# Kernel tuning notes

Hardware: AMD Instinct MI355X
Metric: run time of the kernel (lower is better)

Reference implementation:

```python
import jax, jax.numpy as jnp
import numpy as np

B, N, D = 32, 2048, 1024


def setup_inputs() -> dict:
    key0 = jax.random.key(0)
    ks = jax.random.split(key0, 9)
    scale = 1.0 / np.sqrt(D)
    query = jax.random.normal(ks[0], (B, D), dtype=jnp.float32)
    key = jax.random.normal(ks[1], (B, N, D), dtype=jnp.float32)
    mask = jax.random.randint(ks[2], (B, N), 0, 2, dtype=jnp.int32)
    W1 = jax.random.uniform(ks[3], (D, D), jnp.float32, -scale, scale)
    b1 = jax.random.uniform(ks[4], (D,), jnp.float32, -scale, scale)
    W2 = jax.random.uniform(ks[5], (D, D), jnp.float32, -scale, scale)
    b2 = jax.random.uniform(ks[6], (D,), jnp.float32, -scale, scale)
    v_w = jax.random.uniform(ks[7], (D,), jnp.float32, -scale, scale)
    v_b = jax.random.uniform(ks[8], (), jnp.float32, -scale, scale)
    return {"query": query, "key": key, "mask": mask,
            "W1": W1, "b1": b1, "W2": W2, "b2": b2, "v_w": v_w, "v_b": v_b}


def reference(query, key, mask, W1, b1, W2, b2, v_w, v_b):
    # key_out: [B, N, D] = key @ W1^T + b1 (nn.Linear convention)
    key_out = jnp.einsum('bnd,ed->bne', key, W1) + b1
    # query_out: [B, D] -> broadcast over N
    query_out = jnp.einsum('bd,ed->be', query, W2) + b2
    h = jnp.tanh(key_out + query_out[:, None, :])  # [B, N, D]
    ui = jnp.einsum('bnd,d->bn', h, v_w) + v_b      # v: D -> 1, squeezed
    ui = jnp.where(mask.astype(bool), ui, -jnp.inf)
    return ui
```

## Files before the change

kernel.cpp:

```cpp
#include <hip/hip_runtime.h>
#include <hip/hip_bf16.h>
#include <math.h>

#define B_ 32
#define N_ 2048
#define D_ 1024
#define M_ (B_ * N_)

typedef float  fx4  __attribute__((ext_vector_type(4)));
typedef __bf16 bf16x8 __attribute__((ext_vector_type(8)));
typedef unsigned short us4 __attribute__((ext_vector_type(4)));
typedef unsigned short us8 __attribute__((ext_vector_type(8)));

#define WS_T 2097152ULL

#define MASK_NEG_SENTINEL (-1.0e30f)

__device__ inline unsigned short f2b(float f) {
    __hip_bfloat16 h = __float2bfloat16(f);
    return *reinterpret_cast<unsigned short*>(&h);
}

__global__ void w1_convert_kernel(const fx4* __restrict__ W1,
                                  us4* __restrict__ w1b4) {
    int idx = blockIdx.x * blockDim.x + threadIdx.x;
#pragma unroll
    for (int i = 0; i < 4; ++i) {
        int j = idx + i * 65536;
        fx4 v = W1[j];
        us4 o; o.x = f2b(v.x); o.y = f2b(v.y); o.z = f2b(v.z); o.w = f2b(v.w);
        w1b4[j] = o;
    }
}

__global__ void tq_kernel(const float* __restrict__ query,
                          const float* __restrict__ W2,
                          const float* __restrict__ b1,
                          const float* __restrict__ b2,
                          float* __restrict__ t) {
    int tid = threadIdx.x;
    int p = blockIdx.x * 32 + (tid >> 3);
    int j = tid & 7;
    int b = p >> 10;
    int e = p & 1023;
    const fx4* q = (const fx4*)query + (size_t)b * 256;
    const fx4* w = (const fx4*)W2 + (size_t)e * 256;
    float acc = 0.f;
#pragma unroll 4
    for (int it = 0; it < 32; ++it) {
        int k4 = it * 8 + j;
        fx4 qv = q[k4];
        fx4 wv = w[k4];
        acc += qv.x * wv.x + qv.y * wv.y + qv.z * wv.z + qv.w * wv.w;
    }
    acc += __shfl_xor(acc, 1);
    acc += __shfl_xor(acc, 2);
    acc += __shfl_xor(acc, 4);
    if (j == 0) t[p] = acc + b1[e] + b2[e];
}

__device__ inline float fast_tanh(float x) {
    float ax = fabsf(x);
    float e  = __expf(-2.0f * ax);
    float r  = (1.0f - e) / (1.0f + e);
    return copysignf(r, x);
}

#define BM 64
#define WNC 64
#define NCHUNK 2

__global__ void __launch_bounds__(512)
fused_main(const float* __restrict__ key,
           const unsigned short* __restrict__ w1b,
           const float* __restrict__ t,
           const float* __restrict__ v_w,
           const float* __restrict__ v_b,
           const int* __restrict__ mask,
           float* __restrict__ out) {
    __shared__ unsigned short As[BM * D_];
    __shared__ float rs[8][BM];

    const int tid  = threadIdx.x;
    const int lane = tid & 63;
    const int wave = tid >> 6;
    const int quad = lane >> 4;
    const int l15  = lane & 15;
    const int m0   = blockIdx.x * BM;

    {
#pragma unroll
        for (int r8 = 0; r8 < 8; ++r8) {
            const int row = wave * 8 + r8;
            const fx4* src = (const fx4*)(key + (size_t)(m0 + row) * D_);
#pragma unroll
            for (int p = 0; p < 2; ++p) {
                const int s = p * 64 + lane;
                fx4 v0 = src[s * 2];
                fx4 v1 = src[s * 2 + 1];
                us8 o;
                o[0] = f2b(v0.x); o[1] = f2b(v0.y);
                o[2] = f2b(v0.z); o[3] = f2b(v0.w);
                o[4] = f2b(v1.x); o[5] = f2b(v1.y);
                o[6] = f2b(v1.z); o[7] = f2b(v1.w);
                const int ss = s ^ (row & 7);
                *(us8*)((char*)As + row * 2048 + ss * 16) = o;
            }
        }
    }
    __syncthreads();

    const int b_idx = m0 >> 11;
    const float* trow = t + (size_t)b_idx * D_;
    float rsum[4][4] = {};

    for (int c = 0; c < NCHUNK; ++c) {
        const int e0 = wave * (WNC * NCHUNK) + c * WNC;
        fx4 acc[4][4] = {};
        const unsigned short* bptr =
            w1b + (size_t)(e0 + l15) * D_ + quad * 8;

        for (int k0 = 0; k0 < D_; k0 += 32) {
            bf16x8 a[4], b[4];
#pragma unroll
            for (int j = 0; j < 4; ++j)
                b[j] = *(const bf16x8*)(bptr + (size_t)j * 16 * D_ + k0);
#pragma unroll
            for (int i = 0; i < 4; ++i) {
                const int row  = i * 16 + l15;
                const int slot = ((k0 >> 3) + quad) ^ (row & 7);
                a[i] = *(const bf16x8*)((const char*)As + row * 2048 + slot * 16);
            }
#pragma unroll
            for (int i = 0; i < 4; ++i)
#pragma unroll
                for (int j = 0; j < 4; ++j)
                    acc[i][j] = __builtin_amdgcn_mfma_f32_16x16x32_bf16(
                        a[i], b[j], acc[i][j], 0, 0, 0);
        }

        float vwv[4], tqv[4];
#pragma unroll
        for (int j = 0; j < 4; ++j) {
            const int e = e0 + j * 16 + l15;
            vwv[j] = v_w[e];
            tqv[j] = trow[e];
        }
#pragma unroll
        for (int i = 0; i < 4; ++i)
#pragma unroll
            for (int r = 0; r < 4; ++r) {
                float s = 0.f;
#pragma unroll
                for (int j = 0; j < 4; ++j)
                    s += vwv[j] * fast_tanh(acc[i][j][r] + tqv[j]);
                rsum[i][r] += s;
            }
    }

#pragma unroll
    for (int i = 0; i < 4; ++i)
#pragma unroll
        for (int r = 0; r < 4; ++r) {
            float s = rsum[i][r];
            s += __shfl_xor(s, 1);
            s += __shfl_xor(s, 2);
            s += __shfl_xor(s, 4);
            s += __shfl_xor(s, 8);
            if (l15 == 0) rs[wave][i * 16 + quad * 4 + r] = s;
        }
    __syncthreads();

    if (tid < BM) {
        float u = 0.f;
#pragma unroll
        for (int w = 0; w < 8; ++w) u += rs[w][tid];
        const int m = m0 + tid;
        out[m] = mask[m] ? (u + v_b[0]) : MASK_NEG_SENTINEL;
    }
}

extern "C" void kernel_launch(void* const* d_in, const int* in_sizes, int n_in,
                              void* d_out, int out_size, void* d_ws, size_t ws_size,
                              hipStream_t stream) {
    const float* query = (const float*)d_in[0];
    const float* key   = (const float*)d_in[1];
    const int*   mask  = (const int*)d_in[2];
    const float* W1    = (const float*)d_in[3];
    const float* b1    = (const float*)d_in[4];
    const float* W2    = (const float*)d_in[5];
    const float* b2    = (const float*)d_in[6];
    const float* v_w   = (const float*)d_in[7];
    const float* v_b   = (const float*)d_in[8];

    char* ws = (char*)d_ws;
    unsigned short* w1b = (unsigned short*)ws;
    float*          t   = (float*)(ws + WS_T);

    w1_convert_kernel<<<256, 256, 0, stream>>>((const fx4*)W1, (us4*)w1b);
    tq_kernel<<<1024, 256, 0, stream>>>(query, W2, b1, b2, t);
    fused_main<<<M_ / BM, 512, 0, stream>>>(key, w1b, t, v_w, v_b, mask,
                                            (float*)d_out);
}
```

Baseline: 627.2 us.

## Double-buffer K-slices of W1 and key in LDS with async global-to-LDS loads

Replaces the full-row key staging with a K-streamed loop that double-buffers 32-wide slices of both the bf16 W1 tile and the converted key tile in LDS. W1 slices use global_load_lds so the copy overlaps MFMA work. The block grows to 16 waves, each owning 64 output features, which removes the per-wave chunk loop. It trades per-step block-wide barriers for overlapping global latency with compute.

```diff
diff --git a/kernel.cpp b/kernel.cpp
--- a/kernel.cpp
+++ b/kernel.cpp
@@ -8,9 +8,9 @@
 #define M_ (B_ * N_)
 
 typedef float  fx4  __attribute__((ext_vector_type(4)));
+typedef float  fx2  __attribute__((ext_vector_type(2)));
 typedef __bf16 bf16x8 __attribute__((ext_vector_type(8)));
 typedef unsigned short us4 __attribute__((ext_vector_type(4)));
-typedef unsigned short us8 __attribute__((ext_vector_type(8)));
 
 #define WS_T 2097152ULL
 
@@ -67,10 +67,14 @@
 }
 
 #define BM 64
-#define WNC 64
-#define NCHUNK 2
-
-__global__ void __launch_bounds__(512)
+#define BK 32
+
+#define GLD16(g, l)                                                        \
+    __builtin_amdgcn_global_load_lds(                                      \
+        (const __attribute__((address_space(1))) void*)(g),                \
+        (__attribute__((address_space(3))) void*)(l), 16, 0, 0)
+
+__global__ void __launch_bounds__(1024, 4)
 fused_main(const float* __restrict__ key,
            const unsigned short* __restrict__ w1b,
            const float* __restrict__ t,
@@ -78,8 +82,9 @@
            const float* __restrict__ v_b,
            const int* __restrict__ mask,
            float* __restrict__ out) {
-    __shared__ unsigned short As[BM * D_];
-    __shared__ float rs[8][BM];
+    __shared__ unsigned short Bs[2][D_ * BK];
+    __shared__ unsigned short As[2][BM * BK];
+    __shared__ float rs[16][BM];
 
     const int tid  = threadIdx.x;
     const int lane = tid & 63;
@@ -88,81 +93,97 @@
     const int l15  = lane & 15;
     const int m0   = blockIdx.x * BM;
 
+    const int sB  = (lane & 7) ^ (lane >> 3);
+    const int eL  = ((lane >> 3) << 1) | (sB >> 2);
+    const int ksB = sB & 3;
+    const unsigned short* bsrc =
+        w1b + (size_t)(wave * 64 + eL) * D_ + ksB * 8;
+
+    const int arow = tid >> 4;
+    const int akk  = tid & 15;
+    const float* asrc = key + (size_t)(m0 + arow) * D_ + akk * 2;
+    const int aP  = arow >> 1;
+    const int asl = (((arow & 1) << 2) | (akk >> 2)) ^ (aP & 7);
+    const int aDstOff = aP * 128 + asl * 16 + (akk & 3) * 4;
+
+    int aOff[4], bOff[4];
+#pragma unroll
+    for (int i = 0; i < 4; ++i) {
+        int row = i * 16 + l15;
+        aOff[i] = (row >> 1) * 128 +
+                  ((((row & 1) << 2) | quad) ^ ((row >> 1) & 7)) * 16;
+    }
+#pragma unroll
+    for (int j = 0; j < 4; ++j) {
+        int e = wave * 64 + j * 16 + l15;
+        bOff[j] = (e >> 1) * 128 +
+                  ((((e & 1) << 2) | quad) ^ ((e >> 1) & 7)) * 16;
+    }
+
+    fx4 acc[4][4] = {};
+
     {
-#pragma unroll
-        for (int r8 = 0; r8 < 8; ++r8) {
-            const int row = wave * 8 + r8;
-            const fx4* src = (const fx4*)(key + (size_t)(m0 + row) * D_);
-#pragma unroll
-            for (int p = 0; p < 2; ++p) {
-                const int s = p * 64 + lane;
-                fx4 v0 = src[s * 2];
-                fx4 v1 = src[s * 2 + 1];
-                us8 o;
-                o[0] = f2b(v0.x); o[1] = f2b(v0.y);
-                o[2] = f2b(v0.z); o[3] = f2b(v0.w);
-                o[4] = f2b(v1.x); o[5] = f2b(v1.y);
-                o[6] = f2b(v1.z); o[7] = f2b(v1.w);
-                const int ss = s ^ (row & 7);
-                *(us8*)((char*)As + row * 2048 + ss * 16) = o;
-            }
+        char* bd = (char*)Bs[0] + wave * 4096;
+#pragma unroll
+        for (int q = 0; q < 4; ++q)
+            GLD16(bsrc + q * 16 * D_, bd + q * 1024);
+        fx2 v = *(const fx2*)asrc;
+        unsigned int pk = f2b(v.x) | ((unsigned int)f2b(v.y) << 16);
+        *(unsigned int*)((char*)As[0] + aDstOff) = pk;
+    }
+    __syncthreads();
+
+    int cur = 0;
+    for (int tt = 0; tt < 32; ++tt) {
+        const int k0n = (tt + 1) * BK;
+        fx2 vA;
+        const bool pf = (tt < 31);
+        if (pf) {
+            char* bd = (char*)Bs[cur ^ 1] + wave * 4096;
+#pragma unroll
+            for (int q = 0; q < 4; ++q)
+                GLD16(bsrc + q * 16 * D_ + k0n, bd + q * 1024);
+            vA = *(const fx2*)(asrc + k0n);
         }
-    }
-    __syncthreads();
-
-    const int b_idx = m0 >> 11;
-    const float* trow = t + (size_t)b_idx * D_;
-    float rsum[4][4] = {};
-
-    for (int c = 0; c < NCHUNK; ++c) {
-        const int e0 = wave * (WNC * NCHUNK) + c * WNC;
-        fx4 acc[4][4] = {};
-        const unsigned short* bptr =
-            w1b + (size_t)(e0 + l15) * D_ + quad * 8;
-
-        for (int k0 = 0; k0 < D_; k0 += 32) {
-            bf16x8 a[4], b[4];
+
+        bf16x8 a[4], b[4];
+#pragma unroll
+        for (int i = 0; i < 4; ++i)
+            a[i] = *(const bf16x8*)((const char*)As[cur] + aOff[i]);
+#pragma unroll
+        for (int j = 0; j < 4; ++j)
+            b[j] = *(const bf16x8*)((const char*)Bs[cur] + bOff[j]);
+#pragma unroll
+        for (int i = 0; i < 4; ++i)
 #pragma unroll
             for (int j = 0; j < 4; ++j)
-                b[j] = *(const bf16x8*)(bptr + (size_t)j * 16 * D_ + k0);
-#pragma unroll
-            for (int i = 0; i < 4; ++i) {
-                const int row  = i * 16 + l15;
-                const int slot = ((k0 >> 3) + quad) ^ (row & 7);
-                a[i] = *(const bf16x8*)((const char*)As + row * 2048 + slot * 16);
-            }
-#pragma unroll
-            for (int i = 0; i < 4; ++i)
-#pragma unroll
-                for (int j = 0; j < 4; ++j)
-                    acc[i][j] = __builtin_amdgcn_mfma_f32_16x16x32_bf16(
-                        a[i], b[j], acc[i][j], 0, 0, 0);
+                acc[i][j] = __builtin_amdgcn_mfma_f32_16x16x32_bf16(
+                    a[i], b[j], acc[i][j], 0, 0, 0);
+
+        if (pf) {
+            unsigned int pk = f2b(vA.x) | ((unsigned int)f2b(vA.y) << 16);
+            *(unsigned int*)((char*)As[cur ^ 1] + aDstOff) = pk;
         }
-
-        float vwv[4], tqv[4];
-#pragma unroll
-        for (int j = 0; j < 4; ++j) {
-            const int e = e0 + j * 16 + l15;
-            vwv[j] = v_w[e];
-            tqv[j] = trow[e];
-        }
-#pragma unroll
-        for (int i = 0; i < 4; ++i)
-#pragma unroll
-            for (int r = 0; r < 4; ++r) {
-                float s = 0.f;
-#pragma unroll
-                for (int j = 0; j < 4; ++j)
-                    s += vwv[j] * fast_tanh(acc[i][j][r] + tqv[j]);
-                rsum[i][r] += s;
-            }
-    }
-
+        __syncthreads();
+        cur ^= 1;
+    }
+
+    const float* trow = t + (size_t)(m0 >> 11) * D_;
+    float vwv[4], tqv[4];
+#pragma unroll
+    for (int j = 0; j < 4; ++j) {
+        int e = wave * 64 + j * 16 + l15;
+        vwv[j] = v_w[e];
+        tqv[j] = trow[e];
+    }
 #pragma unroll
     for (int i = 0; i < 4; ++i)
 #pragma unroll
         for (int r = 0; r < 4; ++r) {
-            float s = rsum[i][r];
+            float s = 0.f;
+#pragma unroll
+            for (int j = 0; j < 4; ++j)
+                s += vwv[j] * fast_tanh(acc[i][j][r] + tqv[j]);
             s += __shfl_xor(s, 1);
             s += __shfl_xor(s, 2);
             s += __shfl_xor(s, 4);
@@ -174,7 +195,7 @@
     if (tid < BM) {
         float u = 0.f;
 #pragma unroll
-        for (int w = 0; w < 8; ++w) u += rs[w][tid];
+        for (int w = 0; w < 16; ++w) u += rs[w][tid];
         const int m = m0 + tid;
         out[m] = mask[m] ? (u + v_b[0]) : MASK_NEG_SENTINEL;
     }
@@ -199,6 +220,6 @@
 
     w1_convert_kernel<<<256, 256, 0, stream>>>((const fx4*)W1, (us4*)w1b);
     tq_kernel<<<1024, 256, 0, stream>>>(query, W2, b1, b2, t);
-    fused_main<<<M_ / BM, 512, 0, stream>>>(key, w1b, t, v_w, v_b, mask,
-                                            (float*)d_out);
-}
+    fused_main<<<M_ / BM, 1024, 0, stream>>>(key, w1b, t, v_w, v_b, mask,
+                                             (float*)d_out);
+}
```

Result: no change. 618.1 us (-1.5%).

## Split D output across blocks with double-buffered K-streaming and atomic reduction

Applied to the files above, without the earlier changes.

The main kernel now has each 256-thread block compute a 64-row tile against a quarter of the output features (256 columns). It streams the key operand through two small 32-wide LDS buffers with register prefetch and bf16 conversion, and raises MFMA priority during the multiply. Per-row partial sums go to a zeroed workspace via atomicAdd, and a finalize kernel applies the mask and bias. Weight conversion, the query projection and accumulator zeroing are merged into one prep launch. This cuts LDS use per block, raising occupancy and overlapping loads with compute. The cost is that each key tile is re-read four times, plus the atomics and an extra launch.

```diff
diff --git a/kernel.cpp b/kernel.cpp
--- a/kernel.cpp
+++ b/kernel.cpp
@@ -12,7 +12,8 @@
 typedef unsigned short us4 __attribute__((ext_vector_type(4)));
 typedef unsigned short us8 __attribute__((ext_vector_type(8)));
 
-#define WS_T 2097152ULL
+#define WS_T   2097152ULL
+#define WS_ACC 2228224ULL
 
 #define MASK_NEG_SENTINEL (-1.0e30f)
 
@@ -21,42 +22,50 @@
     return *reinterpret_cast<unsigned short*>(&h);
 }
 
-__global__ void w1_convert_kernel(const fx4* __restrict__ W1,
-                                  us4* __restrict__ w1b4) {
-    int idx = blockIdx.x * blockDim.x + threadIdx.x;
-#pragma unroll
-    for (int i = 0; i < 4; ++i) {
-        int j = idx + i * 65536;
-        fx4 v = W1[j];
-        us4 o; o.x = f2b(v.x); o.y = f2b(v.y); o.z = f2b(v.z); o.w = f2b(v.w);
-        w1b4[j] = o;
-    }
-}
-
-__global__ void tq_kernel(const float* __restrict__ query,
-                          const float* __restrict__ W2,
-                          const float* __restrict__ b1,
-                          const float* __restrict__ b2,
-                          float* __restrict__ t) {
-    int tid = threadIdx.x;
-    int p = blockIdx.x * 32 + (tid >> 3);
-    int j = tid & 7;
-    int b = p >> 10;
-    int e = p & 1023;
-    const fx4* q = (const fx4*)query + (size_t)b * 256;
-    const fx4* w = (const fx4*)W2 + (size_t)e * 256;
-    float acc = 0.f;
+__global__ void prep_kernel(const fx4* __restrict__ W1,
+                            us4* __restrict__ w1b4,
+                            const float* __restrict__ query,
+                            const float* __restrict__ W2,
+                            const float* __restrict__ b1,
+                            const float* __restrict__ b2,
+                            float* __restrict__ t,
+                            fx4* __restrict__ accz) {
+    const int bid = blockIdx.x;
+    const int tid = threadIdx.x;
+    if (bid < 256) {
+        int idx = bid * 256 + tid;
+#pragma unroll
+        for (int i = 0; i < 4; ++i) {
+            int j = idx + i * 65536;
+            fx4 v = W1[j];
+            us4 o; o.x = f2b(v.x); o.y = f2b(v.y);
+            o.z = f2b(v.z); o.w = f2b(v.w);
+            w1b4[j] = o;
+        }
+    } else if (bid < 1280) {
+        int p = (bid - 256) * 32 + (tid >> 3);
+        int j = tid & 7;
+        int b = p >> 10;
+        int e = p & 1023;
+        const fx4* q = (const fx4*)query + (size_t)b * 256;
+        const fx4* w = (const fx4*)W2 + (size_t)e * 256;
+        float acc = 0.f;
 #pragma unroll 4
-    for (int it = 0; it < 32; ++it) {
-        int k4 = it * 8 + j;
-        fx4 qv = q[k4];
-        fx4 wv = w[k4];
-        acc += qv.x * wv.x + qv.y * wv.y + qv.z * wv.z + qv.w * wv.w;
-    }
-    acc += __shfl_xor(acc, 1);
-    acc += __shfl_xor(acc, 2);
-    acc += __shfl_xor(acc, 4);
-    if (j == 0) t[p] = acc + b1[e] + b2[e];
+        for (int it = 0; it < 32; ++it) {
+            int k4 = it * 8 + j;
+            fx4 qv = q[k4];
+            fx4 wv = w[k4];
+            acc += qv.x * wv.x + qv.y * wv.y + qv.z * wv.z + qv.w * wv.w;
+        }
+        acc += __shfl_xor(acc, 1);
+        acc += __shfl_xor(acc, 2);
+        acc += __shfl_xor(acc, 4);
+        if (j == 0) t[p] = acc + b1[e] + b2[e];
+    } else {
+        int idx = (bid - 1280) * 256 + tid;
+        fx4 z = {0.f, 0.f, 0.f, 0.f};
+        accz[idx] = z;
+    }
 }
 
 __device__ inline float fast_tanh(float x) {
@@ -67,102 +76,133 @@
 }
 
 #define BM 64
-#define WNC 64
-#define NCHUNK 2
-
-__global__ void __launch_bounds__(512)
+#define BK 32
+
+__global__ void __launch_bounds__(256, 3)
 fused_main(const float* __restrict__ key,
            const unsigned short* __restrict__ w1b,
            const float* __restrict__ t,
            const float* __restrict__ v_w,
-           const float* __restrict__ v_b,
-           const int* __restrict__ mask,
-           float* __restrict__ out) {
-    __shared__ unsigned short As[BM * D_];
-    __shared__ float rs[8][BM];
+           float* __restrict__ accum) {
+    __shared__ unsigned short As0[BM * BK];
+    __shared__ unsigned short As1[BM * BK];
+    __shared__ float rs[4][BM];
 
     const int tid  = threadIdx.x;
     const int lane = tid & 63;
     const int wave = tid >> 6;
     const int quad = lane >> 4;
     const int l15  = lane & 15;
-    const int m0   = blockIdx.x * BM;
+
+    const int p_ = blockIdx.x;
+    const int mt = (p_ >> 5) * 8 + (p_ & 7);
+    const int hh = (p_ >> 3) & 3;
+    const int m0 = mt * BM;
+    const int eb = hh * 256;
+
+    const unsigned short* bbase =
+        w1b + (size_t)(eb + wave * 64 + l15) * D_ + quad * 8;
+
+    const int arow = tid >> 2;
+    const int akq  = tid & 3;
+    const float* asrc = key + (size_t)(m0 + arow) * D_ + akq * 8;
+    const int aP  = arow >> 1;
+    const int asl = (((arow & 1) << 2) | akq) ^ (aP & 7);
+    const int aDstOff = aP * 128 + asl * 16;
+
+    int aOff[4];
+#pragma unroll
+    for (int i = 0; i < 4; ++i) {
+        int row = i * 16 + l15;
+        aOff[i] = (row >> 1) * 128 +
+                  ((((row & 1) << 2) | quad) ^ ((row >> 1) & 7)) * 16;
+    }
+
+    fx4 acc[4][4] = {};
+    bf16x8 b0[4], b1[4];
+    fx4 aN1lo, aN1hi, aN2lo, aN2hi;
 
     {
 #pragma unroll
-        for (int r8 = 0; r8 < 8; ++r8) {
-            const int row = wave * 8 + r8;
-            const fx4* src = (const fx4*)(key + (size_t)(m0 + row) * D_);
-#pragma unroll
-            for (int p = 0; p < 2; ++p) {
-                const int s = p * 64 + lane;
-                fx4 v0 = src[s * 2];
-                fx4 v1 = src[s * 2 + 1];
-                us8 o;
-                o[0] = f2b(v0.x); o[1] = f2b(v0.y);
-                o[2] = f2b(v0.z); o[3] = f2b(v0.w);
-                o[4] = f2b(v1.x); o[5] = f2b(v1.y);
-                o[6] = f2b(v1.z); o[7] = f2b(v1.w);
-                const int ss = s ^ (row & 7);
-                *(us8*)((char*)As + row * 2048 + ss * 16) = o;
-            }
-        }
-    }
-    __syncthreads();
-
-    const int b_idx = m0 >> 11;
-    const float* trow = t + (size_t)b_idx * D_;
-    float rsum[4][4] = {};
-
-    for (int c = 0; c < NCHUNK; ++c) {
-        const int e0 = wave * (WNC * NCHUNK) + c * WNC;
-        fx4 acc[4][4] = {};
-        const unsigned short* bptr =
-            w1b + (size_t)(e0 + l15) * D_ + quad * 8;
-
-        for (int k0 = 0; k0 < D_; k0 += 32) {
-            bf16x8 a[4], b[4];
+        for (int j = 0; j < 4; ++j)
+            b0[j] = *(const bf16x8*)(bbase + (size_t)j * 16 * D_);
+#pragma unroll
+        for (int j = 0; j < 4; ++j)
+            b1[j] = *(const bf16x8*)(bbase + (size_t)j * 16 * D_ + BK);
+        fx4 v0lo = *(const fx4*)(asrc);
+        fx4 v0hi = *(const fx4*)(asrc + 4);
+        aN1lo = *(const fx4*)(asrc + BK);
+        aN1hi = *(const fx4*)(asrc + BK + 4);
+        aN2lo = *(const fx4*)(asrc + 2 * BK);
+        aN2hi = *(const fx4*)(asrc + 2 * BK + 4);
+        us8 o;
+        o[0] = f2b(v0lo.x); o[1] = f2b(v0lo.y);
+        o[2] = f2b(v0lo.z); o[3] = f2b(v0lo.w);
+        o[4] = f2b(v0hi.x); o[5] = f2b(v0hi.y);
+        o[6] = f2b(v0hi.z); o[7] = f2b(v0hi.w);
+        *(us8*)((char*)As0 + aDstOff) = o;
+        asm volatile("s_waitcnt lgkmcnt(0)" ::: "memory");
+        __builtin_amdgcn_s_barrier();
+        asm volatile("" ::: "memory");
+    }
+
+#define STEP(AsP, AsQ, BB, T)                                              \
+    {                                                                      \
+        us8 o_;                                                            \
+        o_[0] = f2b(aN1lo.x); o_[1] = f2b(aN1lo.y);                        \
+        o_[2] = f2b(aN1lo.z); o_[3] = f2b(aN1lo.w);                        \
+        o_[4] = f2b(aN1hi.x); o_[5] = f2b(aN1hi.y);                        \
+        o_[6] = f2b(aN1hi.z); o_[7] = f2b(aN1hi.w);                        \
+        *(us8*)((char*)(AsQ) + aDstOff) = o_;                              \
+        aN1lo = aN2lo; aN1hi = aN2hi;                                      \
+        int ka_ = (T) + 3; if (ka_ > 31) ka_ = 31;                         \
+        aN2lo = *(const fx4*)(asrc + (size_t)ka_ * BK);                    \
+        aN2hi = *(const fx4*)(asrc + (size_t)ka_ * BK + 4);                \
+        bf16x8 a_[4];                                                      \
+        _Pragma("unroll")                                                  \
+        for (int i_ = 0; i_ < 4; ++i_)                                     \
+            a_[i_] = *(const bf16x8*)((const char*)(AsP) + aOff[i_]);      \
+        __builtin_amdgcn_s_setprio(1);                                     \
+        _Pragma("unroll")                                                  \
+        for (int i_ = 0; i_ < 4; ++i_) {                                   \
+            _Pragma("unroll")                                              \
+            for (int j_ = 0; j_ < 4; ++j_)                                 \
+                acc[i_][j_] = __builtin_amdgcn_mfma_f32_16x16x32_bf16(     \
+                    a_[i_], BB[j_], acc[i_][j_], 0, 0, 0);                 \
+        }                                                                  \
+        __builtin_amdgcn_s_setprio(0);                                     \
+        int kb_ = (T) + 2; if (kb_ > 31) kb_ = 31;                         \
+        _Pragma("unroll")                                                  \
+        for (int j_ = 0; j_ < 4; ++j_)                                     \
+            BB[j_] = *(const bf16x8*)(bbase + (size_t)j_ * 16 * D_ +       \
+                                      (size_t)kb_ * BK);                   \
+        asm volatile("s_waitcnt lgkmcnt(0)" ::: "memory");                 \
+        __builtin_amdgcn_s_barrier();                                      \
+        asm volatile("" ::: "memory");                                     \
+    }
+
+    for (int tt = 0; tt < 32; tt += 2) {
+        STEP(As0, As1, b0, tt);
+        STEP(As1, As0, b1, tt + 1);
+    }
+#undef STEP
+
+    const float* trow = t + (size_t)(m0 >> 11) * D_;
+    float vwv[4], tqv[4];
+#pragma unroll
+    for (int j = 0; j < 4; ++j) {
+        int e = eb + wave * 64 + j * 16 + l15;
+        vwv[j] = v_w[e];
+        tqv[j] = trow[e];
+    }
+#pragma unroll
+    for (int i = 0; i < 4; ++i)
+#pragma unroll
+        for (int r = 0; r < 4; ++r) {
+            float s = 0.f;
 #pragma unroll
             for (int j = 0; j < 4; ++j)
-                b[j] = *(const bf16x8*)(bptr + (size_t)j * 16 * D_ + k0);
-#pragma unroll
-            for (int i = 0; i < 4; ++i) {
-                const int row  = i * 16 + l15;
-                const int slot = ((k0 >> 3) + quad) ^ (row & 7);
-                a[i] = *(const bf16x8*)((const char*)As + row * 2048 + slot * 16);
-            }
-#pragma unroll
-            for (int i = 0; i < 4; ++i)
-#pragma unroll
-                for (int j = 0; j < 4; ++j)
-                    acc[i][j] = __builtin_amdgcn_mfma_f32_16x16x32_bf16(
-                        a[i], b[j], acc[i][j], 0, 0, 0);
-        }
-
-        float vwv[4], tqv[4];
-#pragma unroll
-        for (int j = 0; j < 4; ++j) {
-            const int e = e0 + j * 16 + l15;
-            vwv[j] = v_w[e];
-            tqv[j] = trow[e];
-        }
-#pragma unroll
-        for (int i = 0; i < 4; ++i)
-#pragma unroll
-            for (int r = 0; r < 4; ++r) {
-                float s = 0.f;
-#pragma unroll
-                for (int j = 0; j < 4; ++j)
-                    s += vwv[j] * fast_tanh(acc[i][j][r] + tqv[j]);
-                rsum[i][r] += s;
-            }
-    }
-
-#pragma unroll
-    for (int i = 0; i < 4; ++i)
-#pragma unroll
-        for (int r = 0; r < 4; ++r) {
-            float s = rsum[i][r];
+                s += vwv[j] * fast_tanh(acc[i][j][r] + tqv[j]);
             s += __shfl_xor(s, 1);
             s += __shfl_xor(s, 2);
             s += __shfl_xor(s, 4);
@@ -172,11 +212,19 @@
     __syncthreads();
 
     if (tid < BM) {
-        float u = 0.f;
-#pragma unroll
-        for (int w = 0; w < 8; ++w) u += rs[w][tid];
-        const int m = m0 + tid;
-        out[m] = mask[m] ? (u + v_b[0]) : MASK_NEG_SENTINEL;
+        float u = rs[0][tid] + rs[1][tid] + rs[2][tid] + rs[3][tid];
+        atomicAdd(&accum[m0 + tid], u);
+    }
+}
+
+__global__ void finalize_kernel(const float* __restrict__ accum,
+                                const int* __restrict__ mask,
+                                const float* __restrict__ v_b,
+                                float* __restrict__ out) {
+    int i = blockIdx.x * blockDim.x + threadIdx.x;
+    if (i < M_) {
+        float vb = v_b[0];
+        out[i] = mask[i] ? (accum[i] + vb) : MASK_NEG_SENTINEL;
     }
 }
 
@@ -196,9 +244,11 @@
     char* ws = (char*)d_ws;
     unsigned short* w1b = (unsigned short*)ws;
     float*          t   = (float*)(ws + WS_T);
-
-    w1_convert_kernel<<<256, 256, 0, stream>>>((const fx4*)W1, (us4*)w1b);
-    tq_kernel<<<1024, 256, 0, stream>>>(query, W2, b1, b2, t);
-    fused_main<<<M_ / BM, 512, 0, stream>>>(key, w1b, t, v_w, v_b, mask,
-                                            (float*)d_out);
-}
+    float*          acc = (float*)(ws + WS_ACC);
+
+    prep_kernel<<<1344, 256, 0, stream>>>((const fx4*)W1, (us4*)w1b,
+                                          query, W2, b1, b2, t, (fx4*)acc);
+    fused_main<<<4096, 256, 0, stream>>>(key, w1b, t, v_w, acc);
+    finalize_kernel<<<M_ / 256, 256, 0, stream>>>(acc, mask, v_b,
+                                                  (float*)d_out);
+}
```

After: 626.4 us. Within noise of the previous version (-0.1%).
